# Optimization experiments

Hardware: AMD Instinct MI355X
Metric: run time of the kernel (lower is better)

Reference implementation:

```python
import jax, jax.numpy as jnp
import numpy as np

B = 4096          # batch_size * world_size
D = 256           # embedding dim
TEMP = 0.5        # temperature
EPS = 1e-8


def setup_inputs() -> dict:
    key = jax.random.key(0)
    k1, k2 = jax.random.split(key)
    z_i = jax.random.normal(k1, (B, D), dtype=jnp.float32)
    z_j = jax.random.normal(k2, (B, D), dtype=jnp.float32)
    return {"z_i": z_i, "z_j": z_j}


def reference(z_i, z_j):
    N = 2 * B
    z = jnp.concatenate([z_i, z_j], axis=0)                      # [N, D]
    # cosine similarity = normalized dot products (normalize + GEMM)
    norm = jnp.sqrt(jnp.sum(z * z, axis=-1, keepdims=True))
    zn = z / jnp.maximum(norm, EPS)
    sim = (zn @ zn.T) / TEMP                                     # [N, N]
    # positives: pairs (i, i+B) and (i+B, i)
    idx = jnp.arange(N)
    pos = sim[idx, (idx + B) % N]                                # [N]
    # CE with label 0 over [pos, negatives]; the candidate set equals the
    # full sim row minus the diagonal (pos is re-included), so:
    sim_masked = jnp.where(jnp.eye(N, dtype=bool), -jnp.inf, sim)
    lse = jax.nn.logsumexp(sim_masked, axis=1)                   # [N]
    loss = jnp.sum(lse - pos) / N                                # reduction='sum' then /N
    return loss
```

## Files before the change

### kernel.cpp

```cpp
#include <hip/hip_runtime.h>
#include <hip/hip_bf16.h>
#include <cmath>

#define B_SZ 4096
#define N_SZ 8192
#define D_SZ 256
#define EPS 1e-8f
#define EXPC 0.01127105500694503f
#define EXPB -2.8853900817779268f

typedef __attribute__((ext_vector_type(4))) float f32x4;
typedef __attribute__((ext_vector_type(4))) int   i32x4;
typedef __attribute__((ext_vector_type(8))) int   i32x8;


__global__ __launch_bounds__(256) void prep_kernel(const float* __restrict__ zi,
                                                   const float* __restrict__ zj,
                                                   char* __restrict__ znb,
                                                   float* __restrict__ pos) {
    const int wave = threadIdx.x >> 6, lane = threadIdx.x & 63;
    const int i = blockIdx.x * 4 + wave;
    float4 a = reinterpret_cast<const float4*>(zi + (size_t)i * D_SZ)[lane];
    float4 b = reinterpret_cast<const float4*>(zj + (size_t)i * D_SZ)[lane];
    float ssa = a.x * a.x + a.y * a.y + a.z * a.z + a.w * a.w;
    float ssb = b.x * b.x + b.y * b.y + b.z * b.z + b.w * b.w;
    float dab = a.x * b.x + a.y * b.y + a.z * b.z + a.w * b.w;
    #pragma unroll
    for (int off = 32; off; off >>= 1) {
        ssa += __shfl_xor(ssa, off, 64);
        ssb += __shfl_xor(ssb, off, 64);
        dab += __shfl_xor(dab, off, 64);
    }
    const float invna = 1.0f / fmaxf(sqrtf(ssa), EPS);
    const float invnb = 1.0f / fmaxf(sqrtf(ssb), EPS);
    if (lane == 0) {
        float p = dab * invna * invnb * 2.0f;
        pos[i] = p;
        pos[i + B_SZ] = p;
    }
    const float sa = invna * 16.0f, sb = invnb * 16.0f;
    const int koff = (lane >> 2) * 1024 + (lane & 3) * 4;
    {
        int pk = __builtin_amdgcn_cvt_pk_fp8_f32(a.x * sa, a.y * sa, 0, false);
        pk     = __builtin_amdgcn_cvt_pk_fp8_f32(a.z * sa, a.w * sa, pk, true);
        *reinterpret_cast<int*>(znb + (size_t)(i >> 6) * 16384 + koff + (i & 63) * 16) = pk;
    }
    {
        const int r = i + B_SZ;
        int pk = __builtin_amdgcn_cvt_pk_fp8_f32(b.x * sb, b.y * sb, 0, false);
        pk     = __builtin_amdgcn_cvt_pk_fp8_f32(b.z * sb, b.w * sb, pk, true);
        *reinterpret_cast<int*>(znb + (size_t)(r >> 6) * 16384 + koff + (r & 63) * 16) = pk;
    }
}

__global__ __launch_bounds__(256, 3) void simlse_kernel(const char* __restrict__ znb,
                                                        float* __restrict__ partial) {
    const int t = threadIdx.x;
    const int wave = t >> 6, lane = t & 63;
    const int rt = blockIdx.x >> 5;
    const int chunk = blockIdx.x & 31;
    if (rt > chunk) return;
    const bool offdiag = (rt != chunk);
    __shared__ float cs[4][256];

    const int rl = lane & 15;
    const int kg = lane >> 4;
    const int i0 = rt * 256 + wave * 64;

    const char* ap = znb + (size_t)(rt * 4 + wave) * 16384 + rl * 16;
    i32x8 afrag[4][2];
    #pragma unroll
    for (int g = 0; g < 4; ++g)
        #pragma unroll
        for (int kc = 0; kc < 2; ++kc) {
            i32x4 lo = *reinterpret_cast<const i32x4*>(
                ap + (kc * 8 + kg * 2) * 1024 + g * 256);
            i32x4 hi = *reinterpret_cast<const i32x4*>(
                ap + (kc * 8 + kg * 2 + 1) * 1024 + g * 256);
            afrag[g][kc] = __builtin_shufflevector(lo, hi, 0, 1, 2, 3, 4, 5, 6, 7);
        }

    float s_acc[4][4];
    #pragma unroll
    for (int g = 0; g < 4; ++g)
        #pragma unroll
        for (int r = 0; r < 4; ++r) s_acc[g][r] = 0.0f;

    const char* bp0 = znb + (size_t)chunk * 4 * 16384 + kg * 2048 + rl * 16;

    i32x4 nb0 = *reinterpret_cast<const i32x4*>(bp0);
    i32x4 nb1 = *reinterpret_cast<const i32x4*>(bp0 + 1024);
    i32x4 nb2 = *reinterpret_cast<const i32x4*>(bp0 + 8192);
    i32x4 nb3 = *reinterpret_cast<const i32x4*>(bp0 + 9216);

    #pragma unroll 1
    for (int f = 0; f < 16; ++f) {
        i32x8 bf0 = __builtin_shufflevector(nb0, nb1, 0, 1, 2, 3, 4, 5, 6, 7);
        i32x8 bf1 = __builtin_shufflevector(nb2, nb3, 0, 1, 2, 3, 4, 5, 6, 7);
        if (f < 15) {
            const char* bq = bp0 + ((f + 1) >> 2) * 16384 + ((f + 1) & 3) * 256;
            nb0 = *reinterpret_cast<const i32x4*>(bq);
            nb1 = *reinterpret_cast<const i32x4*>(bq + 1024);
            nb2 = *reinterpret_cast<const i32x4*>(bq + 8192);
            nb3 = *reinterpret_cast<const i32x4*>(bq + 9216);
        }
        f32x4 acc[4];
        #pragma unroll
        for (int g = 0; g < 4; ++g) acc[g] = (f32x4){0.f, 0.f, 0.f, 0.f};
        #pragma unroll
        for (int g = 0; g < 4; ++g)
            asm("v_mfma_f32_16x16x128_f8f6f4 %0, %1, %2, %0"
                : "+v"(acc[g]) : "v"(afrag[g][0]), "v"(bf0));
        #pragma unroll
        for (int g = 0; g < 4; ++g)
            asm("v_mfma_f32_16x16x128_f8f6f4 %0, %1, %2, %0"
                : "+v"(acc[g]) : "v"(afrag[g][1]), "v"(bf1));
        asm volatile("s_nop 7");
        float cthr = 0.0f;
        #pragma unroll
        for (int g = 0; g < 4; ++g)
            #pragma unroll
            for (int r = 0; r < 4; ++r) {
                float e = __builtin_amdgcn_exp2f(fmaf(acc[g][r], EXPC, EXPB));
                s_acc[g][r] += e;
                cthr += e;
            }
        cthr += __shfl_xor(cthr, 16, 64);
        cthr += __shfl_xor(cthr, 32, 64);
        if (offdiag && lane < 16)
            cs[wave][(f >> 2) * 64 + (f & 3) * 16 + rl] = cthr;
    }

    #pragma unroll
    for (int g = 0; g < 4; ++g)
        #pragma unroll
        for (int r = 0; r < 4; ++r) {
            float v = s_acc[g][r];
            #pragma unroll
            for (int off = 1; off < 16; off <<= 1) v += __shfl_xor(v, off, 64);
            if (rl == 0)
                partial[chunk * N_SZ + i0 + g * 16 + kg * 4 + r] = v;
        }

    if (offdiag) {
        __syncthreads();
        float v = cs[0][t] + cs[1][t] + cs[2][t] + cs[3][t];
        partial[rt * N_SZ + chunk * 256 + t] = v;
    }
}

__global__ __launch_bounds__(256) void rowsum_kernel(const float* __restrict__ partial,
                                                     const float* __restrict__ pos,
                                                     float* __restrict__ bpart) {
    const int row = blockIdx.x * 256 + threadIdx.x;
    float s = -1.0f;
    #pragma unroll
    for (int c = 0; c < 32; ++c) s += partial[c * N_SZ + row];
    float acc = 2.0f + logf(s) - pos[row];
    #pragma unroll
    for (int off = 32; off; off >>= 1) acc += __shfl_xor(acc, off, 64);
    __shared__ float w[4];
    if ((threadIdx.x & 63) == 0) w[threadIdx.x >> 6] = acc;
    __syncthreads();
    if (threadIdx.x == 0) bpart[blockIdx.x] = w[0] + w[1] + w[2] + w[3];
}

__global__ __launch_bounds__(64) void finsum_kernel(const float* __restrict__ bpart,
                                                    float* __restrict__ out) {
    float v = threadIdx.x < 32 ? bpart[threadIdx.x] : 0.0f;
    #pragma unroll
    for (int off = 32; off; off >>= 1) v += __shfl_xor(v, off, 64);
    if (threadIdx.x == 0) out[0] = v / (float)N_SZ;
}

extern "C" void kernel_launch(void* const* d_in, const int* in_sizes, int n_in,
                              void* d_out, int out_size, void* d_ws, size_t ws_size,
                              hipStream_t stream) {
    const float* zi = (const float*)d_in[0];
    const float* zj = (const float*)d_in[1];

    char* ws = (char*)d_ws;
    char* znb      = ws;
    float* pos     = (float*)(ws + 2097152);
    float* partial = (float*)(ws + 2097152 + 32768);
    float* bpart   = (float*)(ws + 2097152 + 32768 + 1048576);
    float* out = (float*)d_out;

    prep_kernel<<<B_SZ / 4, 256, 0, stream>>>(zi, zj, znb, pos);
    simlse_kernel<<<1024, 256, 0, stream>>>(znb, partial);
    rowsum_kernel<<<32, 256, 0, stream>>>(partial, pos, bpart);
    finsum_kernel<<<1, 64, 0, stream>>>(bpart, out);
}
```

Baseline: 38.89 us.

## Software-pipeline MFMA and exp with double accumulators; launch only upper-triangle tiles

Double-buffers the MFMA accumulators so the exp/sum work for one 16-column tile overlaps with the matrix multiplies of the next tile. The grid now launches only the 528 upper-triangular blocks, decoding row/chunk with a short loop, instead of 1024 blocks where half exit early. Launch bounds drop from 3 to 2 blocks per SM to make room for the extra accumulator registers, which may cost occupancy.

```diff
diff --git a/kernel.cpp b/kernel.cpp
--- a/kernel.cpp
+++ b/kernel.cpp
@@ -53,13 +53,19 @@
     }
 }
 
-__global__ __launch_bounds__(256, 3) void simlse_kernel(const char* __restrict__ znb,
+__global__ __launch_bounds__(256, 2) void simlse_kernel(const char* __restrict__ znb,
                                                         float* __restrict__ partial) {
     const int t = threadIdx.x;
     const int wave = t >> 6, lane = t & 63;
-    const int rt = blockIdx.x >> 5;
-    const int chunk = blockIdx.x & 31;
-    if (rt > chunk) return;
+
+    int bid = blockIdx.x, rt = 0;
+    #pragma unroll 1
+    for (; rt < 32; ++rt) {
+        int cnt = 32 - rt;
+        if (bid < cnt) break;
+        bid -= cnt;
+    }
+    const int chunk = rt + bid;
     const bool offdiag = (rt != chunk);
     __shared__ float cs[4][256];
 
@@ -93,43 +99,71 @@
     i32x4 nb2 = *reinterpret_cast<const i32x4*>(bp0 + 8192);
     i32x4 nb3 = *reinterpret_cast<const i32x4*>(bp0 + 9216);
 
+    i32x8 bf0, bf1;
+    f32x4 accA[4], accB[4];
+
+    #define PREP_B(F)                                                             \
+        {                                                                         \
+            bf0 = __builtin_shufflevector(nb0, nb1, 0, 1, 2, 3, 4, 5, 6, 7);      \
+            bf1 = __builtin_shufflevector(nb2, nb3, 0, 1, 2, 3, 4, 5, 6, 7);      \
+            if ((F) < 15) {                                                       \
+                const char* bq = bp0 + (((F) + 1) >> 2) * 16384 +                 \
+                                 (((F) + 1) & 3) * 256;                           \
+                nb0 = *reinterpret_cast<const i32x4*>(bq);                        \
+                nb1 = *reinterpret_cast<const i32x4*>(bq + 1024);                 \
+                nb2 = *reinterpret_cast<const i32x4*>(bq + 8192);                 \
+                nb3 = *reinterpret_cast<const i32x4*>(bq + 9216);                 \
+            }                                                                     \
+        }
+
+    #define MFMA8(ACC)                                                            \
+        {                                                                         \
+            _Pragma("unroll")                                                     \
+            for (int g = 0; g < 4; ++g) ACC[g] = (f32x4){0.f, 0.f, 0.f, 0.f};     \
+            _Pragma("unroll")                                                     \
+            for (int g = 0; g < 4; ++g)                                           \
+                asm("v_mfma_f32_16x16x128_f8f6f4 %0, %1, %2, %0"                  \
+                    : "+v"(ACC[g]) : "v"(afrag[g][0]), "v"(bf0));                 \
+            _Pragma("unroll")                                                     \
+            for (int g = 0; g < 4; ++g)                                           \
+                asm("v_mfma_f32_16x16x128_f8f6f4 %0, %1, %2, %0"                  \
+                    : "+v"(ACC[g]) : "v"(afrag[g][1]), "v"(bf1));                 \
+        }
+
+    #define EXPSUM(ACC, F)                                                        \
+        {                                                                         \
+            float cthr = 0.0f;                                                    \
+            _Pragma("unroll")                                                     \
+            for (int g = 0; g < 4; ++g)                                           \
+                _Pragma("unroll")                                                 \
+                for (int r = 0; r < 4; ++r) {                                     \
+                    float e = __builtin_amdgcn_exp2f(fmaf(ACC[g][r], EXPC, EXPB)); \
+                    s_acc[g][r] += e;                                             \
+                    cthr += e;                                                    \
+                }                                                                 \
+            cthr += __shfl_xor(cthr, 16, 64);                                     \
+            cthr += __shfl_xor(cthr, 32, 64);                                     \
+            if (offdiag && lane < 16)                                             \
+                cs[wave][((F) >> 2) * 64 + ((F) & 3) * 16 + rl] = cthr;           \
+        }
+
+    PREP_B(0);
+    MFMA8(accA);
     #pragma unroll 1
-    for (int f = 0; f < 16; ++f) {
-        i32x8 bf0 = __builtin_shufflevector(nb0, nb1, 0, 1, 2, 3, 4, 5, 6, 7);
-        i32x8 bf1 = __builtin_shufflevector(nb2, nb3, 0, 1, 2, 3, 4, 5, 6, 7);
-        if (f < 15) {
-            const char* bq = bp0 + ((f + 1) >> 2) * 16384 + ((f + 1) & 3) * 256;
-            nb0 = *reinterpret_cast<const i32x4*>(bq);
-            nb1 = *reinterpret_cast<const i32x4*>(bq + 1024);
-            nb2 = *reinterpret_cast<const i32x4*>(bq + 8192);
-            nb3 = *reinterpret_cast<const i32x4*>(bq + 9216);
-        }
-        f32x4 acc[4];
-        #pragma unroll
-        for (int g = 0; g < 4; ++g) acc[g] = (f32x4){0.f, 0.f, 0.f, 0.f};
-        #pragma unroll
-        for (int g = 0; g < 4; ++g)
-            asm("v_mfma_f32_16x16x128_f8f6f4 %0, %1, %2, %0"
-                : "+v"(acc[g]) : "v"(afrag[g][0]), "v"(bf0));
-        #pragma unroll
-        for (int g = 0; g < 4; ++g)
-            asm("v_mfma_f32_16x16x128_f8f6f4 %0, %1, %2, %0"
-                : "+v"(acc[g]) : "v"(afrag[g][1]), "v"(bf1));
+    for (int fo = 0; fo < 7; ++fo) {
+        const int f1 = 2 * fo + 1, f2 = 2 * fo + 2;
+        PREP_B(f1); MFMA8(accB);
         asm volatile("s_nop 7");
-        float cthr = 0.0f;
-        #pragma unroll
-        for (int g = 0; g < 4; ++g)
-            #pragma unroll
-            for (int r = 0; r < 4; ++r) {
-                float e = __builtin_amdgcn_exp2f(fmaf(acc[g][r], EXPC, EXPB));
-                s_acc[g][r] += e;
-                cthr += e;
-            }
-        cthr += __shfl_xor(cthr, 16, 64);
-        cthr += __shfl_xor(cthr, 32, 64);
-        if (offdiag && lane < 16)
-            cs[wave][(f >> 2) * 64 + (f & 3) * 16 + rl] = cthr;
-    }
+        EXPSUM(accA, f1 - 1);
+        PREP_B(f2); MFMA8(accA);
+        asm volatile("s_nop 7");
+        EXPSUM(accB, f2 - 1);
+    }
+    PREP_B(15); MFMA8(accB);
+    asm volatile("s_nop 7");
+    EXPSUM(accA, 14);
+    asm volatile("s_nop 7");
+    EXPSUM(accB, 15);
 
     #pragma unroll
     for (int g = 0; g < 4; ++g)
@@ -147,6 +181,9 @@
         float v = cs[0][t] + cs[1][t] + cs[2][t] + cs[3][t];
         partial[rt * N_SZ + chunk * 256 + t] = v;
     }
+    #undef PREP_B
+    #undef MFMA8
+    #undef EXPSUM
 }
 
 __global__ __launch_bounds__(256) void rowsum_kernel(const float* __restrict__ partial,
@@ -187,7 +224,7 @@
     float* out = (float*)d_out;
 
     prep_kernel<<<B_SZ / 4, 256, 0, stream>>>(zi, zj, znb, pos);
-    simlse_kernel<<<1024, 256, 0, stream>>>(znb, partial);
+    simlse_kernel<<<528, 256, 0, stream>>>(znb, partial);
     rowsum_kernel<<<32, 256, 0, stream>>>(partial, pos, bpart);
     finsum_kernel<<<1, 64, 0, stream>>>(bpart, out);
 }
```

New measurement: 35.12 us. -9.7%, faster.
